# Kernel optimization log

Measured on AMD Instinct MI355X. Metric: run time of the kernel, lower is better.

Reference implementation:

```python
import jax, jax.numpy as jnp
import numpy as np

D_IN = 1024
D_OUT = 1024
NUM_HEADS = 16
HEAD_DIM = D_OUT // NUM_HEADS


def setup_inputs() -> dict:
    key = jax.random.key(0)
    ks = jax.random.split(key, 6)
    s = 1.0 / np.sqrt(D_IN)
    return {
        "x": jax.random.normal(ks[0], (4, 2048, D_IN), dtype=jnp.float32),
        "Wq": jax.random.uniform(ks[1], (D_IN, D_OUT), jnp.float32, -s, s),
        "Wk": jax.random.uniform(ks[2], (D_IN, D_OUT), jnp.float32, -s, s),
        "Wv": jax.random.uniform(ks[3], (D_IN, D_OUT), jnp.float32, -s, s),
        "Wo": jax.random.uniform(ks[4], (D_OUT, D_OUT), jnp.float32, -s, s),
        "bo": jax.random.uniform(ks[5], (D_OUT,), jnp.float32, -s, s),
    }


def reference(x, Wq, Wk, Wv, Wo, bo):
    b, n, _ = x.shape
    # QKV projections -> [b, h, n, d]
    def heads(t):
        return t.reshape(b, n, NUM_HEADS, HEAD_DIM).transpose(0, 2, 1, 3)
    q = heads(x @ Wq)
    k = heads(x @ Wk)
    v = heads(x @ Wv)
    # scaled scores with causal mask
    scores = jnp.einsum("bhqd,bhkd->bhqk", q, k) / jnp.sqrt(jnp.float32(HEAD_DIM))
    causal = jnp.tril(jnp.ones((n, n), dtype=bool))  # True = keep
    scores = jnp.where(causal, scores, -jnp.inf)
    attn = jax.nn.softmax(scores, axis=-1)  # dropout p=0.0 -> identity
    ctx = jnp.einsum("bhqk,bhkd->bhqd", attn, v)
    ctx = ctx.transpose(0, 2, 1, 3).reshape(b, n, D_OUT)
    return ctx @ Wo + bo
```

## Files before the change

kernel.cpp:

```cpp
#include <hip/hip_runtime.h>
#include <hip/hip_bf16.h>
#include <math.h>

typedef __attribute__((ext_vector_type(8))) __bf16 bf16x8;
typedef __attribute__((ext_vector_type(4))) __bf16 bf16x4;
typedef __attribute__((ext_vector_type(4))) float f32x4;
typedef __attribute__((ext_vector_type(4))) short short4_t;

#define D_MODEL 1024
#define SEQ     2048
#define BATCH   4
#define NH      16
#define HD      64
#define MROWS   (BATCH * SEQ)

#define SCALE_LOG2E 0.18033688011112042f

__device__ __forceinline__ void gld_lds16(const __bf16* g, __bf16* l) {
  __builtin_amdgcn_global_load_lds(
      (const __attribute__((address_space(1))) void*)g,
      (__attribute__((address_space(3))) void*)l, 16, 0, 0);
}

__global__ __launch_bounds__(256) void cvt_x(const float* __restrict__ in,
                                             __bf16* __restrict__ out) {
  int i = (blockIdx.x * 256 + threadIdx.x) * 4;
  float4 f = *(const float4*)(in + i);
  bf16x4 o;
  o.x = (__bf16)f.x; o.y = (__bf16)f.y; o.z = (__bf16)f.z; o.w = (__bf16)f.w;
  *(bf16x4*)(out + i) = o;
}

__global__ __launch_bounds__(256) void cvt_wt4(const float* __restrict__ W0,
                                               const float* __restrict__ W1,
                                               const float* __restrict__ W2,
                                               const float* __restrict__ W3,
                                               __bf16* __restrict__ Wqkv,
                                               __bf16* __restrict__ Wot) {
  __shared__ __bf16 t[32][33];
  int tx = threadIdx.x, ty = threadIdx.y;
  int z = blockIdx.z;
  const float* W = (z == 0) ? W0 : (z == 1) ? W1 : (z == 2) ? W2 : W3;
  __bf16* Wt = (z < 3) ? (Wqkv + (size_t)z * 1024 * 1024) : Wot;
  int n0 = blockIdx.x * 32, k0 = blockIdx.y * 32;
#pragma unroll
  for (int j = 0; j < 32; j += 8)
    t[ty + j][tx] = (__bf16)W[(size_t)(k0 + ty + j) * D_MODEL + n0 + tx];
  __syncthreads();
#pragma unroll
  for (int j = 0; j < 32; j += 8)
    Wt[(size_t)(n0 + ty + j) * D_MODEL + k0 + tx] = t[tx][ty + j];
}

template <int EPI>
__global__ __launch_bounds__(256) void gemm_bt(const __bf16* __restrict__ A,
                                               const __bf16* __restrict__ Bt,
                                               const float* __restrict__ bias,
                                               void* __restrict__ Cout) {
  constexpr int Kd = 1024;
  constexpr bool SWAP = (EPI != 1);
  constexpr int GX = (EPI == 0) ? 16 : 8;
  __shared__ __bf16 As[128 * 64];
  __shared__ __bf16 Bs[128 * 64];
  const int tid = threadIdx.x;
  const int lane = tid & 63;
  const int w = tid >> 6;
  const int quad = lane >> 4, l16 = lane & 15;
  const int wr = w >> 1, wc = w & 1;

  const int id  = blockIdx.y * GX + blockIdx.x;
  const int nwg = GX * gridDim.y;
  const int wk  = (id & 7) * (nwg >> 3) + (id >> 3);
  const int tm = (wk / GX) * 128, tn = (wk % GX) * 128;

  f32x4 acc[4][4] = {};

  const __bf16* gA[4]; const __bf16* gB[4]; int dst[4];
#pragma unroll
  for (int j = 0; j < 4; ++j) {
    int s = w * 256 + j * 64 + lane;
    int row = (s >> 2) & 127, kk = s >> 9, c = (s & 3) * 8;
    int go = kk * 32 + c;
    gA[j] = A + (size_t)(tm + row) * Kd + go;
    gB[j] = Bt + (size_t)(tn + row) * Kd + go;
    dst[j] = s * 8;
  }

  for (int k0 = 0; k0 < Kd; k0 += 64) {
#pragma unroll
    for (int j = 0; j < 4; ++j) {
      gld_lds16(gA[j] + k0, As + dst[j]);
      gld_lds16(gB[j] + k0, Bs + dst[j]);
    }
    __syncthreads();
#pragma unroll
    for (int kk = 0; kk < 2; ++kk) {
      bf16x8 af[4], bfr[4];
#pragma unroll
      for (int t = 0; t < 4; ++t) {
        af[t]  = *(const bf16x8*)&As[kk * 4096 + (wr * 64 + t * 16 + l16) * 32 + quad * 8];
        bfr[t] = *(const bf16x8*)&Bs[kk * 4096 + (wc * 64 + t * 16 + l16) * 32 + quad * 8];
      }
#pragma unroll
      for (int mt = 0; mt < 4; ++mt)
#pragma unroll
        for (int nt = 0; nt < 4; ++nt) {
          if constexpr (SWAP)
            acc[mt][nt] = __builtin_amdgcn_mfma_f32_16x16x32_bf16(
                bfr[nt], af[mt], acc[mt][nt], 0, 0, 0);
          else
            acc[mt][nt] = __builtin_amdgcn_mfma_f32_16x16x32_bf16(
                af[mt], bfr[nt], acc[mt][nt], 0, 0, 0);
        }
    }
    __syncthreads();
  }

#pragma unroll
  for (int mt = 0; mt < 4; ++mt)
#pragma unroll
    for (int nt = 0; nt < 4; ++nt) {
      if constexpr (EPI == 2) {
        int gm  = tm + wr * 64 + mt * 16 + l16;
        int gn0 = tn + wc * 64 + nt * 16 + quad * 4;
        float4 bv = *(const float4*)&bias[gn0];
        float4 o;
        o.x = acc[mt][nt][0] + bv.x;
        o.y = acc[mt][nt][1] + bv.y;
        o.z = acc[mt][nt][2] + bv.z;
        o.w = acc[mt][nt][3] + bv.w;
        *(float4*)&((float*)Cout)[(size_t)gm * 1024 + gn0] = o;
      } else if constexpr (EPI == 0) {
        int gm = tm + wr * 64 + mt * 16 + l16;
        int f0 = tn + wc * 64 + nt * 16 + quad * 4;
        int which = f0 >> 10, col = f0 & 1023;
        int b = gm >> 11, nn = gm & 2047, h = col >> 6, d = col & 63;
        float s = (which == 0) ? SCALE_LOG2E : 1.0f;
        bf16x4 o;
        o[0] = (__bf16)(acc[mt][nt][0] * s);
        o[1] = (__bf16)(acc[mt][nt][1] * s);
        o[2] = (__bf16)(acc[mt][nt][2] * s);
        o[3] = (__bf16)(acc[mt][nt][3] * s);
        __bf16* op = (__bf16*)Cout + (size_t)which * (BATCH * SEQ * (size_t)D_MODEL) +
                     ((size_t)(b * NH + h) * SEQ + nn) * HD + d;
        *(bf16x4*)op = o;
      } else {
        int gm0 = tm + wr * 64 + mt * 16 + quad * 4;
        int gn  = tn + wc * 64 + nt * 16 + l16;
        int b = gm0 >> 11, nn0 = gm0 & 2047, h = gn >> 6, d = gn & 63;
        bf16x4 o;
        o[0] = (__bf16)acc[mt][nt][0];
        o[1] = (__bf16)acc[mt][nt][1];
        o[2] = (__bf16)acc[mt][nt][2];
        o[3] = (__bf16)acc[mt][nt][3];
        __bf16* op = (__bf16*)Cout + ((size_t)(b * NH + h) * HD + d) * SEQ + nn0;
        *(bf16x4*)op = o;
      }
    }
}

__global__ __launch_bounds__(256, 2) void attn(const __bf16* __restrict__ Q,
                                               const __bf16* __restrict__ K,
                                               const __bf16* __restrict__ Vt,
                                               __bf16* __restrict__ ctx) {
  const int tid = threadIdx.x;
  const int lane = tid & 63, w = tid >> 6;
  const int quad = lane >> 4, l16 = lane & 15;
  const int byy = blockIdx.y;
  const int tile = (byy & 1) ? (15 - (byy >> 1)) : (byy >> 1);
  const int bh = blockIdx.x;
  const __bf16* qb = Q + (size_t)bh * SEQ * HD;
  const __bf16* kb = K + (size_t)bh * SEQ * HD;
  const __bf16* vb = Vt + (size_t)bh * HD * SEQ;

  __shared__ __bf16 KsAll[2 * 4096];
  __shared__ __bf16 VsAll[2 * 4096];

  const int qmin = tile * 128 + w * 32;

  bf16x8 aq[2][2];
#pragma unroll
  for (int qq = 0; qq < 2; ++qq)
#pragma unroll
    for (int kk = 0; kk < 2; ++kk)
      aq[qq][kk] = *(const bf16x8*)(qb + (size_t)(qmin + qq * 16 + l16) * HD +
                                    kk * 32 + quad * 8);

  f32x4 acc[2][4] = {};
  f32x4 sumacc[2] = {};
  const f32x4 fz = {};
  const short bf16_one = (short)0x3F80;
  const short4_t vones = {bf16_one, bf16_one, bf16_one, bf16_one};

  const int u0 = w * 128 + lane;
  const int u1 = u0 + 64;
  const int kOffG0 = ((u0 >> 2) & 63) * HD + (u0 >> 8) * 32 + (u0 & 3) * 8;
  const int kOffG1 = ((u1 >> 2) & 63) * HD + (u1 >> 8) * 32 + (u1 & 3) * 8;
  const int vd0 = u0 >> 3, vd1 = u1 >> 3;
  const int vOffG0 = vd0 * SEQ + (((u0 & 7) ^ (vd0 & 7)) * 8);
  const int vOffG1 = vd1 * SEQ + (((u1 & 7) ^ (vd1 & 7)) * 8);

  auto stage = [&](int k0s, int bufsel) {
    __bf16* Kb = KsAll + bufsel * 4096;
    __bf16* Vb = VsAll + bufsel * 4096;
    gld_lds16(kb + (size_t)k0s * HD + kOffG0, Kb + u0 * 8);
    gld_lds16(kb + (size_t)k0s * HD + kOffG1, Kb + u1 * 8);
    gld_lds16(vb + k0s + vOffG0, Vb + u0 * 8);
    gld_lds16(vb + k0s + vOffG1, Vb + u1 * 8);
  };

  const int nIter = 2 * tile + 2;
  stage(0, 0);

  for (int it = 0; it < nIter; ++it) {
    __syncthreads();
    if (it + 1 < nIter) stage((it + 1) * 64, (it + 1) & 1);

    const int k0 = it * 64;
    if (k0 <= qmin + 31) {
      const __bf16* Kb = KsAll + (it & 1) * 4096;
      const __bf16* Vb = VsAll + (it & 1) * 4096;

      bf16x8 bk[4][2];
#pragma unroll
      for (int kt = 0; kt < 4; ++kt)
#pragma unroll
        for (int kk = 0; kk < 2; ++kk)
          bk[kt][kk] = *(const bf16x8*)&Kb[kk * 2048 + (kt * 16 + l16) * 32 + quad * 8];

      short4_t vf[4][4];
#pragma unroll
      for (int kt = 0; kt < 4; ++kt)
#pragma unroll
        for (int cd = 0; cd < 4; ++cd)
          vf[kt][cd] = *(const short4_t*)&Vb[(cd * 16 + l16) * 64 +
                                             (((kt * 2 + (quad >> 1)) ^ (l16 & 7)) * 8) +
                                             (quad & 1) * 4];

      f32x4 St[4][2];
#pragma unroll
      for (int kt = 0; kt < 4; ++kt)
#pragma unroll
        for (int qq = 0; qq < 2; ++qq) {
          St[kt][qq] = __builtin_amdgcn_mfma_f32_16x16x32_bf16(
              bk[kt][0], aq[qq][0], fz, 0, 0, 0);
          St[kt][qq] = __builtin_amdgcn_mfma_f32_16x16x32_bf16(
              bk[kt][1], aq[qq][1], St[kt][qq], 0, 0, 0);
        }
      const bool full = (k0 + 63 <= qmin);
#pragma unroll
      for (int kt = 0; kt < 4; ++kt)
#pragma unroll
        for (int qq = 0; qq < 2; ++qq) {
          float e0 = __builtin_amdgcn_exp2f(St[kt][qq][0]);
          float e1 = __builtin_amdgcn_exp2f(St[kt][qq][1]);
          float e2 = __builtin_amdgcn_exp2f(St[kt][qq][2]);
          float e3 = __builtin_amdgcn_exp2f(St[kt][qq][3]);
          if (!full) {
            int kg = k0 + kt * 16 + quad * 4;
            int qg = qmin + qq * 16 + l16;
            if (kg + 0 > qg) e0 = 0.f;
            if (kg + 1 > qg) e1 = 0.f;
            if (kg + 2 > qg) e2 = 0.f;
            if (kg + 3 > qg) e3 = 0.f;
          }
          short4_t ap;
          ap[0] = __builtin_bit_cast(short, (__bf16)e0);
          ap[1] = __builtin_bit_cast(short, (__bf16)e1);
          ap[2] = __builtin_bit_cast(short, (__bf16)e2);
          ap[3] = __builtin_bit_cast(short, (__bf16)e3);
          sumacc[qq] = __builtin_amdgcn_mfma_f32_16x16x16bf16_1k(
              ap, vones, sumacc[qq], 0, 0, 0);
#pragma unroll
          for (int cd = 0; cd < 4; ++cd)
            acc[qq][cd] = __builtin_amdgcn_mfma_f32_16x16x16bf16_1k(
                ap, vf[kt][cd], acc[qq][cd], 0, 0, 0);
        }
    }
  }

  const int bb = bh >> 4, hh = bh & 15;
#pragma unroll
  for (int qq = 0; qq < 2; ++qq) {
    float rinv[4];
#pragma unroll
    for (int i = 0; i < 4; ++i)
      rinv[i] = 1.0f / sumacc[qq][i];
#pragma unroll
    for (int c = 0; c < 4; ++c)
#pragma unroll
      for (int i = 0; i < 4; ++i) {
        int q = qmin + qq * 16 + quad * 4 + i;
        float o = acc[qq][c][i] * rinv[i];
        ctx[((size_t)(bb * SEQ + q)) * D_MODEL + hh * HD + c * 16 + l16] = (__bf16)o;
      }
  }
}

extern "C" void kernel_launch(void* const* d_in, const int* in_sizes, int n_in,
                              void* d_out, int out_size, void* d_ws, size_t ws_size,
                              hipStream_t stream) {
  const float* x  = (const float*)d_in[0];
  const float* Wq = (const float*)d_in[1];
  const float* Wk = (const float*)d_in[2];
  const float* Wv = (const float*)d_in[3];
  const float* Wo = (const float*)d_in[4];
  const float* bo = (const float*)d_in[5];
  float* out = (float*)d_out;
  char* ws = (char*)d_ws;
  const size_t MB = 1024 * 1024;
  __bf16* xb   = (__bf16*)(ws);
  __bf16* Wqkv = (__bf16*)(ws + 16 * MB);
  __bf16* Wot  = (__bf16*)(ws + 22 * MB);
  __bf16* Qh   = (__bf16*)(ws + 24 * MB);
  __bf16* Kh   = (__bf16*)(ws + 40 * MB);
  __bf16* Vth  = (__bf16*)(ws + 56 * MB);
  __bf16* ctx  = xb;

  cvt_x<<<MROWS * D_MODEL / (256 * 4), 256, 0, stream>>>(x, xb);
  cvt_wt4<<<dim3(32, 32, 4), dim3(32, 8), 0, stream>>>(Wq, Wk, Wv, Wo, Wqkv, Wot);

  gemm_bt<0><<<dim3(16, 64), 256, 0, stream>>>(xb, Wqkv, nullptr, Qh);
  gemm_bt<1><<<dim3(8, 64), 256, 0, stream>>>(xb, Wqkv + 2 * 1024 * 1024, nullptr, Vth);

  attn<<<dim3(64, 16), 256, 0, stream>>>(Qh, Kh, Vth, ctx);

  gemm_bt<2><<<dim3(8, 64), 256, 0, stream>>>(ctx, Wot, bo, out);
}
```

Before: 255.7 us.

## Add 256x256 double-buffered GEMM kernel for fused Q/K projection

```diff
diff --git a/kernel.cpp b/kernel.cpp
--- a/kernel.cpp
+++ b/kernel.cpp
@@ -52,6 +52,90 @@
     Wt[(size_t)(n0 + ty + j) * D_MODEL + k0 + tx] = t[tx][ty + j];
 }
 
+__global__ __launch_bounds__(512) void gemm256(const __bf16* __restrict__ A,
+                                               const __bf16* __restrict__ Bt,
+                                               __bf16* __restrict__ Cout) {
+  constexpr int Kd = 1024;
+  constexpr int NT = Kd / 64;
+  __shared__ __bf16 As[2][256 * 64];
+  __shared__ __bf16 Bs[2][256 * 64];
+  const int tid = threadIdx.x;
+  const int lane = tid & 63;
+  const int w = tid >> 6;
+  const int quad = lane >> 4, l16 = lane & 15;
+  const int wr = w >> 2, wc = w & 3;
+
+  const int id  = blockIdx.y * 8 + blockIdx.x;
+  const int wk  = (id & 7) * 32 + (id >> 3);
+  const int tm = (wk >> 3) * 256, tn = (wk & 7) * 256;
+
+  f32x4 acc[8][4] = {};
+
+  const __bf16* gA[4]; const __bf16* gB[4]; int dst[4];
+#pragma unroll
+  for (int j = 0; j < 4; ++j) {
+    int s = j * 512 + tid;
+    int row = (s >> 2) & 255, kk = s >> 10, c = (s & 3) * 8;
+    int go = kk * 32 + c;
+    gA[j] = A + (size_t)(tm + row) * Kd + go;
+    gB[j] = Bt + (size_t)(tn + row) * Kd + go;
+    dst[j] = s * 8;
+  }
+
+  auto stage = [&](int k0s, int bf) {
+#pragma unroll
+    for (int j = 0; j < 4; ++j) {
+      gld_lds16(gA[j] + k0s, &As[bf][dst[j]]);
+      gld_lds16(gB[j] + k0s, &Bs[bf][dst[j]]);
+    }
+  };
+
+  stage(0, 0);
+  __syncthreads();
+
+  int buf = 0;
+  for (int t = 0; t < NT; ++t) {
+    if (t + 1 < NT) stage((t + 1) * 64, buf ^ 1);
+#pragma unroll
+    for (int kk = 0; kk < 2; ++kk) {
+      bf16x8 af[8], bfr[4];
+#pragma unroll
+      for (int x = 0; x < 8; ++x)
+        af[x] = *(const bf16x8*)&As[buf][kk * 8192 + (wr * 128 + x * 16 + l16) * 32 + quad * 8];
+#pragma unroll
+      for (int y = 0; y < 4; ++y)
+        bfr[y] = *(const bf16x8*)&Bs[buf][kk * 8192 + (wc * 64 + y * 16 + l16) * 32 + quad * 8];
+#pragma unroll
+      for (int mt = 0; mt < 8; ++mt)
+#pragma unroll
+        for (int nt = 0; nt < 4; ++nt)
+          acc[mt][nt] = __builtin_amdgcn_mfma_f32_16x16x32_bf16(
+              bfr[nt], af[mt], acc[mt][nt], 0, 0, 0);
+    }
+    __syncthreads();
+    buf ^= 1;
+  }
+
+#pragma unroll
+  for (int mt = 0; mt < 8; ++mt)
+#pragma unroll
+    for (int nt = 0; nt < 4; ++nt) {
+      int gm = tm + wr * 128 + mt * 16 + l16;
+      int f0 = tn + wc * 64 + nt * 16 + quad * 4;
+      int which = f0 >> 10, col = f0 & 1023;
+      int b = gm >> 11, nn = gm & 2047, h = col >> 6, d = col & 63;
+      float s = (which == 0) ? SCALE_LOG2E : 1.0f;
+      bf16x4 o;
+      o[0] = (__bf16)(acc[mt][nt][0] * s);
+      o[1] = (__bf16)(acc[mt][nt][1] * s);
+      o[2] = (__bf16)(acc[mt][nt][2] * s);
+      o[3] = (__bf16)(acc[mt][nt][3] * s);
+      __bf16* op = Cout + (size_t)which * (BATCH * SEQ * (size_t)D_MODEL) +
+                   ((size_t)(b * NH + h) * SEQ + nn) * HD + d;
+      *(bf16x4*)op = o;
+    }
+}
+
 template <int EPI>
 __global__ __launch_bounds__(256) void gemm_bt(const __bf16* __restrict__ A,
                                                const __bf16* __restrict__ Bt,
@@ -59,7 +143,7 @@
                                                void* __restrict__ Cout) {
   constexpr int Kd = 1024;
   constexpr bool SWAP = (EPI != 1);
-  constexpr int GX = (EPI == 0) ? 16 : 8;
+  constexpr int GX = 8;
   __shared__ __bf16 As[128 * 64];
   __shared__ __bf16 Bs[128 * 64];
   const int tid = threadIdx.x;
@@ -130,20 +214,6 @@
         o.z = acc[mt][nt][2] + bv.z;
         o.w = acc[mt][nt][3] + bv.w;
         *(float4*)&((float*)Cout)[(size_t)gm * 1024 + gn0] = o;
-      } else if constexpr (EPI == 0) {
-        int gm = tm + wr * 64 + mt * 16 + l16;
-        int f0 = tn + wc * 64 + nt * 16 + quad * 4;
-        int which = f0 >> 10, col = f0 & 1023;
-        int b = gm >> 11, nn = gm & 2047, h = col >> 6, d = col & 63;
-        float s = (which == 0) ? SCALE_LOG2E : 1.0f;
-        bf16x4 o;
-        o[0] = (__bf16)(acc[mt][nt][0] * s);
-        o[1] = (__bf16)(acc[mt][nt][1] * s);
-        o[2] = (__bf16)(acc[mt][nt][2] * s);
-        o[3] = (__bf16)(acc[mt][nt][3] * s);
-        __bf16* op = (__bf16*)Cout + (size_t)which * (BATCH * SEQ * (size_t)D_MODEL) +
-                     ((size_t)(b * NH + h) * SEQ + nn) * HD + d;
-        *(bf16x4*)op = o;
       } else {
         int gm0 = tm + wr * 64 + mt * 16 + quad * 4;
         int gn  = tn + wc * 64 + nt * 16 + l16;
@@ -320,7 +390,7 @@
   cvt_x<<<MROWS * D_MODEL / (256 * 4), 256, 0, stream>>>(x, xb);
   cvt_wt4<<<dim3(32, 32, 4), dim3(32, 8), 0, stream>>>(Wq, Wk, Wv, Wo, Wqkv, Wot);
 
-  gemm_bt<0><<<dim3(16, 64), 256, 0, stream>>>(xb, Wqkv, nullptr, Qh);
+  gemm256<<<dim3(8, 32), 512, 0, stream>>>(xb, Wqkv, Qh);
   gemm_bt<1><<<dim3(8, 64), 256, 0, stream>>>(xb, Wqkv + 2 * 1024 * 1024, nullptr, Vth);
 
   attn<<<dim3(64, 16), 256, 0, stream>>>(Qh, Kh, Vth, ctx);
```

After: 252.1 us. Within noise of the previous version (-1.4%).
